# Kernel tuning notes

Measured on AMD Instinct MI355X. Metric: run time of the kernel, lower is better.

Reference implementation:

```python
import jax, jax.numpy as jnp
import numpy as np

SOLVER_STEPS = 4  # fixed-step Euler steps per ODE solve (solver_step)


def setup_inputs() -> dict:
    key = jax.random.key(0)
    ks = jax.random.split(key, 10)
    B, T, D, H = 256, 1024, 128, 512
    sd = 1.0 / np.sqrt(H)
    n = lambda k, shape, scale: (jax.random.normal(k, shape, jnp.float32) * scale)
    return {
        "x": n(ks[0], (B, T, D), 1.0),
        "t": jax.random.uniform(ks[1], (B, T, 1), jnp.float32),
        # torch.nn.LSTMCell parameters (gate order: input, forget, cell, output)
        "W_ih": n(ks[2], (4 * H, D), sd),
        "W_hh": n(ks[3], (4 * H, H), sd),
        "b_ih": n(ks[4], (4 * H,), sd),
        "b_hh": n(ks[5], (4 * H,), sd),
        # DiffeqConcat drift MLP: (H+1) -> H -> H, Tanh activation
        "w1": n(ks[6], (H, H + 1), 1.0 / np.sqrt(H + 1)),
        "b1": n(ks[7], (H,), 0.01),
        "w2": n(ks[8], (H, H), sd),
        "b2": n(ks[9], (H,), 0.01),
    }


def _drift(y, s, w1, b1, w2, b2):
    # MLP(concat([s, y])): s is the (scalar) integration time in [0, 1]
    inp = jnp.concatenate([jnp.full_like(y[..., :1], s), y], axis=-1)
    return jnp.tanh(inp @ w1.T + b1) @ w2.T + b2


def _ode_evolve(h, t_i, w1, b1, w2, b2):
    # Integrate dy/ds = t_i * f(s, y) for s in [0, 1] with fixed-step Euler
    # (torchdiffeq time-rescaling trick used by ODEModel/DiffeqConcat).
    dt = 1.0 / SOLVER_STEPS
    y = h
    for k in range(SOLVER_STEPS):
        y = y + dt * t_i * _drift(y, k * dt, w1, b1, w2, b2)  # t_i: (B,1) broadcasts
    return y


def _lstm_cell(x_i, c, h, W_ih, W_hh, b_ih, b_hh):
    gates = x_i @ W_ih.T + b_ih + h @ W_hh.T + b_hh  # (B, 4H)
    i, f, g, o = jnp.split(gates, 4, axis=-1)
    c_new = jax.nn.sigmoid(f) * c + jax.nn.sigmoid(i) * jnp.tanh(g)
    h_new = jax.nn.sigmoid(o) * jnp.tanh(c_new)
    return c_new, h_new


def reference(x, t, W_ih, W_hh, b_ih, b_hh, w1, b1, w2, b2):
    B, T, D = x.shape
    H = W_hh.shape[1]

    def step(carry, inp):
        c, h = carry
        x_i, t_i = inp  # (B, D), (B, 1)
        h_pre = _ode_evolve(h, t_i, w1, b1, w2, b2)
        c, h = _lstm_cell(x_i, c, h, W_ih, W_hh, b_ih, b_hh)
        return (c, h), h_pre

    init = (jnp.zeros((B, H), x.dtype), jnp.zeros((B, H), x.dtype))
    xs = (jnp.swapaxes(x, 0, 1), jnp.swapaxes(t, 0, 1))  # time-major for scan
    _, hiddens = jax.lax.scan(step, init, xs)  # (T, B, H)
    return jnp.swapaxes(hiddens, 0, 1)  # (B, T, H)
```

## Files before the change

### kernel.cpp

```cpp
#include <hip/hip_runtime.h>
#include <stdint.h>

#define B_  256
#define T_  1024
#define D_  128
#define H_  512
#define G4_ 2048
#define BT_ (B_ * T_)

#define NG_  16
#define NCW_ 8

typedef unsigned short u16;
typedef __attribute__((ext_vector_type(8))) short    bf16x8;
typedef __attribute__((ext_vector_type(8))) u16      u16x8;
typedef __attribute__((ext_vector_type(4))) float    f32x4;
typedef __attribute__((ext_vector_type(4))) uint32_t u32x4;

static __device__ __forceinline__ u16 f2bf(float f) {
  uint32_t u = __builtin_bit_cast(uint32_t, f);
  u += 0x7FFFu + ((u >> 16) & 1u);
  return (u16)(u >> 16);
}

static __device__ __forceinline__ u16x8 pack8(float4 a, float4 b) {
  u16x8 p;
  p[0] = f2bf(a.x); p[1] = f2bf(a.y); p[2] = f2bf(a.z); p[3] = f2bf(a.w);
  p[4] = f2bf(b.x); p[5] = f2bf(b.y); p[6] = f2bf(b.z); p[7] = f2bf(b.w);
  return p;
}

static __device__ __forceinline__ float fast_sig(float x) {
  return 1.f / (1.f + __expf(-x));
}
static __device__ __forceinline__ float fast_tanh(float x) {
  return 1.f - 2.f / (__expf(2.f * x) + 1.f);
}

__global__ void prep_kernel(const float* __restrict__ Whh, const float* __restrict__ Wih,
                            const float* __restrict__ w1,  const float* __restrict__ w2,
                            const float* __restrict__ b_ih, const float* __restrict__ b_hh,
                            u16* __restrict__ Whh_bf, u16* __restrict__ Wih_bf,
                            u16* __restrict__ w1y_bf, u16* __restrict__ w2_bf,
                            float* __restrict__ w1s, float* __restrict__ bsum,
                            uint32_t* __restrict__ xch32, float* __restrict__ Yd) {
  const int idx = blockIdx.x * blockDim.x + threadIdx.x;
  if (idx < G4_ * H_) Whh_bf[idx] = f2bf(Whh[idx]);
  if (idx < G4_ * D_) Wih_bf[idx] = f2bf(Wih[idx]);
  if (idx < H_ * H_) {
    const int n = idx >> 9, k = idx & 511;
    w1y_bf[idx] = f2bf(w1[n * 513 + 1 + k]);
    w2_bf[idx]  = f2bf(w2[idx]);
  }
  if (idx < H_)  w1s[idx]  = w1[idx * 513];
  if (idx < G4_) bsum[idx] = b_ih[idx] + b_hh[idx];
  if (idx < 2 * B_ * H_) xch32[idx] = 0;
  if (idx < B_ * H_) {
    const int b = idx >> 9, h = idx & 511;
    Yd[(size_t)b * T_ * H_ + h] = 0.f;
  }
}

__global__ void xconv_kernel(const float* __restrict__ x, u16* __restrict__ xbf) {
  const size_t i = ((size_t)blockIdx.x * blockDim.x + threadIdx.x) * 16;
  const float4* s4 = (const float4*)(x + i);
  float4 a = s4[0], b = s4[1], c = s4[2], d = s4[3];
  *(u16x8*)(xbf + i)     = pack8(a, b);
  *(u16x8*)(xbf + i + 8) = pack8(c, d);
}

__launch_bounds__(256, 1)
__global__ void lstm_persist5(const u16* __restrict__ xbf,
                              const u16* __restrict__ Whh_bf,
                              const u16* __restrict__ Wih_bf,
                              const float* __restrict__ bsum,
                              float* __restrict__ Yd,
                              uint32_t* __restrict__ xch32) {
  __shared__ u16 As[16][648];

  const int tid  = threadIdx.x;
  const int lane = tid & 63;
  const int wv   = tid >> 6;
  const int bid  = blockIdx.x;
  const int g    = bid & 15;
  const int cw   = bid >> 4;
  const int br0  = g * 16;

  const int cl = lane & 15;
  const int ko = (lane >> 4) * 8;
  const int jb = cw * 64 + wv * 16 + cl;

  bf16x8 wf[4][20];
#pragma unroll
  for (int gt = 0; gt < 4; ++gt) {
    const size_t j0 = (size_t)(gt * H_ + jb);
#pragma unroll
    for (int kt = 0; kt < 16; ++kt)
      wf[gt][kt] = *(const bf16x8*)(Whh_bf + j0 * H_ + kt * 32 + ko);
#pragma unroll
    for (int kt = 0; kt < 4; ++kt)
      wf[gt][16 + kt] = *(const bf16x8*)(Wih_bf + j0 * D_ + kt * 32 + ko);
  }
#pragma unroll
  for (int gt = 0; gt < 4; ++gt)
#pragma unroll
    for (int kt = 0; kt < 20; ++kt)
      asm volatile("" : "+v"(wf[gt][kt]));

  const int row0 = (lane >> 4) * 4;
  float cst[4] = {0.f, 0.f, 0.f, 0.f};
  const float bi  = bsum[jb];
  const float bff = bsum[H_ + jb];
  const float bgg = bsum[2 * H_ + jb];
  const float boo = bsum[3 * H_ + jb];

  const int prow = tid >> 4;
  const int pcb  = (tid & 15) * 32;
  const u16* xrow = xbf + (size_t)(br0 + (tid >> 4)) * T_ * D_ + (tid & 15) * 8;

  for (int s = 0; s < T_ - 1; ++s) {
    const u16x8 xa = *(const u16x8*)(xrow + (size_t)s * D_);

    if (s == 0) {
      u16x8 z = {};
#pragma unroll
      for (int i = 0; i < 4; ++i) *(u16x8*)&As[prow][pcb + i * 8] = z;
    } else {
      const char* base = (const char*)(xch32 + (((size_t)(s & 1) * NG_ + g) << 13)) + tid * 128;
      const uint32_t want = (uint32_t)s;
      u32x4 r0, r1, r2, r3, r4, r5, r6, r7;
      bool ok;
      do {
        asm volatile(
          "global_load_dwordx4 %0, %8, off sc0 sc1\n\t"
          "global_load_dwordx4 %1, %8, off offset:16 sc0 sc1\n\t"
          "global_load_dwordx4 %2, %8, off offset:32 sc0 sc1\n\t"
          "global_load_dwordx4 %3, %8, off offset:48 sc0 sc1\n\t"
          "global_load_dwordx4 %4, %8, off offset:64 sc0 sc1\n\t"
          "global_load_dwordx4 %5, %8, off offset:80 sc0 sc1\n\t"
          "global_load_dwordx4 %6, %8, off offset:96 sc0 sc1\n\t"
          "global_load_dwordx4 %7, %8, off offset:112 sc0 sc1\n\t"
          "s_waitcnt vmcnt(0)"
          : "=&v"(r0), "=&v"(r1), "=&v"(r2), "=&v"(r3),
            "=&v"(r4), "=&v"(r5), "=&v"(r6), "=&v"(r7)
          : "v"(base) : "memory");
        ok = true;
#pragma unroll
        for (int i = 0; i < 4; ++i) {
          ok = ok && ((r0[i] & 0xFFFFu) == want) && ((r1[i] & 0xFFFFu) == want)
                  && ((r2[i] & 0xFFFFu) == want) && ((r3[i] & 0xFFFFu) == want)
                  && ((r4[i] & 0xFFFFu) == want) && ((r5[i] & 0xFFFFu) == want)
                  && ((r6[i] & 0xFFFFu) == want) && ((r7[i] & 0xFFFFu) == want);
        }
      } while (!ok);
      u16x8 d0, d1, d2, d3;
#pragma unroll
      for (int i = 0; i < 4; ++i) {
        d0[i] = (u16)(r0[i] >> 16); d0[4 + i] = (u16)(r1[i] >> 16);
        d1[i] = (u16)(r2[i] >> 16); d1[4 + i] = (u16)(r3[i] >> 16);
        d2[i] = (u16)(r4[i] >> 16); d2[4 + i] = (u16)(r5[i] >> 16);
        d3[i] = (u16)(r6[i] >> 16); d3[4 + i] = (u16)(r7[i] >> 16);
      }
      *(u16x8*)&As[prow][pcb]      = d0;
      *(u16x8*)&As[prow][pcb + 8]  = d1;
      *(u16x8*)&As[prow][pcb + 16] = d2;
      *(u16x8*)&As[prow][pcb + 24] = d3;
    }
    *(u16x8*)&As[tid >> 4][512 + (tid & 15) * 8] = xa;
    __syncthreads();

    f32x4 a0 = {}, a1 = {}, a2 = {}, a3 = {};
#pragma unroll
    for (int kt = 0; kt < 20; ++kt) {
      bf16x8 a = *(const bf16x8*)&As[cl][kt * 32 + ko];
      a0 = __builtin_amdgcn_mfma_f32_16x16x32_bf16(a, wf[0][kt], a0, 0, 0, 0);
      a1 = __builtin_amdgcn_mfma_f32_16x16x32_bf16(a, wf[1][kt], a1, 0, 0, 0);
      a2 = __builtin_amdgcn_mfma_f32_16x16x32_bf16(a, wf[2][kt], a2, 0, 0, 0);
      a3 = __builtin_amdgcn_mfma_f32_16x16x32_bf16(a, wf[3][kt], a3, 0, 0, 0);
    }

    {
      const uint32_t tag = (uint32_t)(s + 1);
      uint32_t* xdst = xch32 + (((size_t)((s + 1) & 1) * NG_ + g) << 13) + row0 * 512 + jb;
      float*    ydst = Yd + ((size_t)(br0 + row0) * T_ + (s + 1)) * H_ + jb;
#pragma unroll
      for (int r = 0; r < 4; ++r) {
        const float gi = a0[r] + bi;
        const float gf = a1[r] + bff;
        const float gg = a2[r] + bgg;
        const float go = a3[r] + boo;
        cst[r] = fast_sig(gf) * cst[r] + fast_sig(gi) * fast_tanh(gg);
        const float h = fast_sig(go) * fast_tanh(cst[r]);
        const uint32_t wd = ((uint32_t)f2bf(h) << 16) | tag;
        asm volatile("global_store_dword %0, %1, off sc0 sc1"
                     :: "v"(xdst + r * 512), "v"(wd) : "memory");
        ydst[(size_t)r * T_ * H_] = h;
      }
    }
    __syncthreads();
  }
}

__launch_bounds__(512)
__global__ void ode_fused2(const float* __restrict__ tptr,
                           const u16* __restrict__ w1y,
                           const u16* __restrict__ w2v,
                           const float* __restrict__ b1,
                           const float* __restrict__ b2,
                           const float* __restrict__ w1s,
                           float* __restrict__ Yd) {
  __shared__ u16 At[64][520];

  const int tid  = threadIdx.x;
  const int lane = tid & 63;
  const int wv   = tid >> 6;
  const int n0w  = wv * 64;
  const size_t m0 = (size_t)blockIdx.x * 64;
  const int cl = lane & 15;
  const int rq = (lane >> 4) * 4;
  const int ko = (lane >> 4) * 8;

  float b1v[4], b2v[4], w1sv[4];
#pragma unroll
  for (int nf = 0; nf < 4; ++nf) {
    const int cg = n0w + nf * 16 + cl;
    b1v[nf] = b1[cg]; b2v[nf] = b2[cg]; w1sv[nf] = w1s[cg];
  }
  float tv[4][4];
#pragma unroll
  for (int mf = 0; mf < 4; ++mf)
#pragma unroll
    for (int r = 0; r < 4; ++r)
      tv[mf][r] = 0.25f * tptr[m0 + mf * 16 + rq + r];

  f32x4 Y[4][4];
#pragma unroll
  for (int mf = 0; mf < 4; ++mf)
#pragma unroll
    for (int nf = 0; nf < 4; ++nf)
#pragma unroll
      for (int r = 0; r < 4; ++r)
        Y[mf][nf][r] = Yd[(m0 + mf * 16 + rq + r) * 512 + n0w + nf * 16 + cl];

#define WRITE_AT(EXPR)                                                        \
  do {                                                                        \
    _Pragma("unroll") for (int mf = 0; mf < 4; ++mf)                          \
    _Pragma("unroll") for (int nf = 0; nf < 4; ++nf)                          \
    _Pragma("unroll") for (int r = 0; r < 4; ++r)                             \
      At[mf * 16 + rq + r][n0w + nf * 16 + cl] = f2bf(EXPR);                  \
  } while (0)

#define GEMM_DIRECT(WPTR, ACC)                                                \
  do {                                                                        \
    _Pragma("unroll 2") for (int cc = 0; cc < 16; ++cc) {                     \
      bf16x8 bfv[4], af[4];                                                   \
      _Pragma("unroll") for (int nf = 0; nf < 4; ++nf)                        \
        bfv[nf] = *(const bf16x8*)((WPTR) + (size_t)(n0w + nf * 16 + cl) * 512\
                                   + cc * 32 + ko);                           \
      _Pragma("unroll") for (int mf = 0; mf < 4; ++mf)                        \
        af[mf] = *(const bf16x8*)&At[mf * 16 + cl][cc * 32 + ko];             \
      _Pragma("unroll") for (int mf = 0; mf < 4; ++mf)                        \
      _Pragma("unroll") for (int nf = 0; nf < 4; ++nf)                        \
        ACC[mf][nf] = __builtin_amdgcn_mfma_f32_16x16x32_bf16(                \
            af[mf], bfv[nf], ACC[mf][nf], 0, 0, 0);                           \
    }                                                                         \
  } while (0)

  WRITE_AT(Y[mf][nf][r]);
  __syncthreads();

#pragma unroll 1
  for (int k = 0; k < 4; ++k) {
    const float sk = 0.25f * k;
    f32x4 acc[4][4] = {};
    GEMM_DIRECT(w1y, acc);
    __syncthreads();
    WRITE_AT(fast_tanh(acc[mf][nf][r] + b1v[nf] + sk * w1sv[nf]));
    __syncthreads();
    f32x4 acc2[4][4] = {};
    GEMM_DIRECT(w2v, acc2);
    __syncthreads();
#pragma unroll
    for (int mf = 0; mf < 4; ++mf)
#pragma unroll
      for (int nf = 0; nf < 4; ++nf)
#pragma unroll
        for (int r = 0; r < 4; ++r)
          Y[mf][nf][r] += tv[mf][r] * (acc2[mf][nf][r] + b2v[nf]);
    if (k < 3) {
      WRITE_AT(Y[mf][nf][r]);
      __syncthreads();
    }
  }
#undef GEMM_DIRECT
#undef WRITE_AT

#pragma unroll
  for (int mf = 0; mf < 4; ++mf)
#pragma unroll
    for (int nf = 0; nf < 4; ++nf)
#pragma unroll
      for (int r = 0; r < 4; ++r)
        Yd[(m0 + mf * 16 + rq + r) * 512 + n0w + nf * 16 + cl] = Y[mf][nf][r];
}

extern "C" void kernel_launch(void* const* d_in, const int* in_sizes, int n_in,
                              void* d_out, int out_size, void* d_ws, size_t ws_size,
                              hipStream_t stream) {
  const float* x    = (const float*)d_in[0];
  const float* t    = (const float*)d_in[1];
  const float* W_ih = (const float*)d_in[2];
  const float* W_hh = (const float*)d_in[3];
  const float* b_ih = (const float*)d_in[4];
  const float* b_hh = (const float*)d_in[5];
  const float* w1   = (const float*)d_in[6];
  const float* b1   = (const float*)d_in[7];
  const float* w2   = (const float*)d_in[8];
  const float* b2   = (const float*)d_in[9];
  float* Yd = (float*)d_out;

  char* ws = (char*)d_ws;
  size_t off = 0;
  auto alloc = [&](size_t bytes) {
    void* p = ws + off;
    off += (bytes + 255) & ~(size_t)255;
    return p;
  };
  u16*      Whh_bf = (u16*)alloc((size_t)G4_ * H_ * 2);
  u16*      Wih_bf = (u16*)alloc((size_t)G4_ * D_ * 2);
  u16*      w1y_bf = (u16*)alloc((size_t)H_ * H_ * 2);
  u16*      w2_bf  = (u16*)alloc((size_t)H_ * H_ * 2);
  float*    w1s    = (float*)alloc(H_ * 4);
  float*    bsum   = (float*)alloc(G4_ * 4);
  uint32_t* xch32  = (uint32_t*)alloc((size_t)2 * B_ * H_ * 4);
  u16*      xbf    = (u16*)alloc((size_t)BT_ * D_ * 2);

  prep_kernel<<<4096, 256, 0, stream>>>(W_hh, W_ih, w1, w2, b_ih, b_hh,
                                        Whh_bf, Wih_bf, w1y_bf, w2_bf, w1s, bsum, xch32, Yd);
  xconv_kernel<<<8192, 256, 0, stream>>>(x, xbf);

  lstm_persist5<<<dim3(NG_ * NCW_), 256, 0, stream>>>(xbf, Whh_bf, Wih_bf, bsum, Yd, xch32);

  ode_fused2<<<dim3(BT_ / 64), 512, 0, stream>>>(t, w1y_bf, w2_bf, b1, b2, w1s, Yd);
}
```

Before: 6.912 ms.

## Duplicate hidden-state exchange into L2-scoped and system-scoped buffers for faster polling

Each LSTM block now writes its tagged hidden state twice: once with an sc0-only store (intended to stay coherent at the local L2/XCD level) and once with an sc0 sc1 store to a second buffer. Consumers poll the sc0-only buffer, which is meant to be cheaper per probe, and every fourth failed spin fall back to the system-coherent copy so cross-XCD producers are still observed. The aim is to cut the latency of the per-step inter-block handoff in the persistent recurrence. The cost is doubled exchange stores and a second workspace buffer. It also depends on the coherence semantics of the cache-scope bits, because peers on another XCD may only be seen through the fallback path.

```diff
diff --git a/kernel.cpp b/kernel.cpp
--- a/kernel.cpp
+++ b/kernel.cpp
@@ -43,7 +43,8 @@
                             u16* __restrict__ Whh_bf, u16* __restrict__ Wih_bf,
                             u16* __restrict__ w1y_bf, u16* __restrict__ w2_bf,
                             float* __restrict__ w1s, float* __restrict__ bsum,
-                            uint32_t* __restrict__ xch32, float* __restrict__ Yd) {
+                            uint32_t* __restrict__ xchL, uint32_t* __restrict__ xchM,
+                            float* __restrict__ Yd) {
   const int idx = blockIdx.x * blockDim.x + threadIdx.x;
   if (idx < G4_ * H_) Whh_bf[idx] = f2bf(Whh[idx]);
   if (idx < G4_ * D_) Wih_bf[idx] = f2bf(Wih[idx]);
@@ -54,7 +55,7 @@
   }
   if (idx < H_)  w1s[idx]  = w1[idx * 513];
   if (idx < G4_) bsum[idx] = b_ih[idx] + b_hh[idx];
-  if (idx < 2 * B_ * H_) xch32[idx] = 0;
+  if (idx < 2 * B_ * H_) { xchL[idx] = 0; xchM[idx] = 0; }
   if (idx < B_ * H_) {
     const int b = idx >> 9, h = idx & 511;
     Yd[(size_t)b * T_ * H_ + h] = 0.f;
@@ -70,12 +71,13 @@
 }
 
 __launch_bounds__(256, 1)
-__global__ void lstm_persist5(const u16* __restrict__ xbf,
+__global__ void lstm_persist6(const u16* __restrict__ xbf,
                               const u16* __restrict__ Whh_bf,
                               const u16* __restrict__ Wih_bf,
                               const float* __restrict__ bsum,
                               float* __restrict__ Yd,
-                              uint32_t* __restrict__ xch32) {
+                              uint32_t* __restrict__ xchL,
+                              uint32_t* __restrict__ xchM) {
   __shared__ u16 As[16][648];
 
   const int tid  = threadIdx.x;
@@ -126,24 +128,27 @@
 #pragma unroll
       for (int i = 0; i < 4; ++i) *(u16x8*)&As[prow][pcb + i * 8] = z;
     } else {
-      const char* base = (const char*)(xch32 + (((size_t)(s & 1) * NG_ + g) << 13)) + tid * 128;
+      const size_t blk = ((size_t)(s & 1) * NG_ + g) << 13;
+      const char* baseL = (const char*)(xchL + blk) + tid * 128;
+      const char* baseM = (const char*)(xchM + blk) + tid * 128;
       const uint32_t want = (uint32_t)s;
       u32x4 r0, r1, r2, r3, r4, r5, r6, r7;
-      bool ok;
+      bool ok = false;
+      int spin = 0;
       do {
         asm volatile(
-          "global_load_dwordx4 %0, %8, off sc0 sc1\n\t"
-          "global_load_dwordx4 %1, %8, off offset:16 sc0 sc1\n\t"
-          "global_load_dwordx4 %2, %8, off offset:32 sc0 sc1\n\t"
-          "global_load_dwordx4 %3, %8, off offset:48 sc0 sc1\n\t"
-          "global_load_dwordx4 %4, %8, off offset:64 sc0 sc1\n\t"
-          "global_load_dwordx4 %5, %8, off offset:80 sc0 sc1\n\t"
-          "global_load_dwordx4 %6, %8, off offset:96 sc0 sc1\n\t"
-          "global_load_dwordx4 %7, %8, off offset:112 sc0 sc1\n\t"
+          "global_load_dwordx4 %0, %8, off sc0\n\t"
+          "global_load_dwordx4 %1, %8, off offset:16 sc0\n\t"
+          "global_load_dwordx4 %2, %8, off offset:32 sc0\n\t"
+          "global_load_dwordx4 %3, %8, off offset:48 sc0\n\t"
+          "global_load_dwordx4 %4, %8, off offset:64 sc0\n\t"
+          "global_load_dwordx4 %5, %8, off offset:80 sc0\n\t"
+          "global_load_dwordx4 %6, %8, off offset:96 sc0\n\t"
+          "global_load_dwordx4 %7, %8, off offset:112 sc0\n\t"
           "s_waitcnt vmcnt(0)"
           : "=&v"(r0), "=&v"(r1), "=&v"(r2), "=&v"(r3),
             "=&v"(r4), "=&v"(r5), "=&v"(r6), "=&v"(r7)
-          : "v"(base) : "memory");
+          : "v"(baseL) : "memory");
         ok = true;
 #pragma unroll
         for (int i = 0; i < 4; ++i) {
@@ -151,6 +156,29 @@
                   && ((r2[i] & 0xFFFFu) == want) && ((r3[i] & 0xFFFFu) == want)
                   && ((r4[i] & 0xFFFFu) == want) && ((r5[i] & 0xFFFFu) == want)
                   && ((r6[i] & 0xFFFFu) == want) && ((r7[i] & 0xFFFFu) == want);
+        }
+        if (!ok && ((spin++ & 3) == 3)) {
+          asm volatile(
+            "global_load_dwordx4 %0, %8, off sc0 sc1\n\t"
+            "global_load_dwordx4 %1, %8, off offset:16 sc0 sc1\n\t"
+            "global_load_dwordx4 %2, %8, off offset:32 sc0 sc1\n\t"
+            "global_load_dwordx4 %3, %8, off offset:48 sc0 sc1\n\t"
+            "global_load_dwordx4 %4, %8, off offset:64 sc0 sc1\n\t"
+            "global_load_dwordx4 %5, %8, off offset:80 sc0 sc1\n\t"
+            "global_load_dwordx4 %6, %8, off offset:96 sc0 sc1\n\t"
+            "global_load_dwordx4 %7, %8, off offset:112 sc0 sc1\n\t"
+            "s_waitcnt vmcnt(0)"
+            : "=&v"(r0), "=&v"(r1), "=&v"(r2), "=&v"(r3),
+              "=&v"(r4), "=&v"(r5), "=&v"(r6), "=&v"(r7)
+            : "v"(baseM) : "memory");
+          ok = true;
+#pragma unroll
+          for (int i = 0; i < 4; ++i) {
+            ok = ok && ((r0[i] & 0xFFFFu) == want) && ((r1[i] & 0xFFFFu) == want)
+                    && ((r2[i] & 0xFFFFu) == want) && ((r3[i] & 0xFFFFu) == want)
+                    && ((r4[i] & 0xFFFFu) == want) && ((r5[i] & 0xFFFFu) == want)
+                    && ((r6[i] & 0xFFFFu) == want) && ((r7[i] & 0xFFFFu) == want);
+          }
         }
       } while (!ok);
       u16x8 d0, d1, d2, d3;
@@ -181,7 +209,9 @@
 
     {
       const uint32_t tag = (uint32_t)(s + 1);
-      uint32_t* xdst = xch32 + (((size_t)((s + 1) & 1) * NG_ + g) << 13) + row0 * 512 + jb;
+      const size_t nblk = ((size_t)((s + 1) & 1) * NG_ + g) << 13;
+      uint32_t* dL = xchL + nblk + row0 * 512 + jb;
+      uint32_t* dM = xchM + nblk + row0 * 512 + jb;
       float*    ydst = Yd + ((size_t)(br0 + row0) * T_ + (s + 1)) * H_ + jb;
 #pragma unroll
       for (int r = 0; r < 4; ++r) {
@@ -192,8 +222,9 @@
         cst[r] = fast_sig(gf) * cst[r] + fast_sig(gi) * fast_tanh(gg);
         const float h = fast_sig(go) * fast_tanh(cst[r]);
         const uint32_t wd = ((uint32_t)f2bf(h) << 16) | tag;
-        asm volatile("global_store_dword %0, %1, off sc0 sc1"
-                     :: "v"(xdst + r * 512), "v"(wd) : "memory");
+        asm volatile("global_store_dword %0, %2, off sc0\n\t"
+                     "global_store_dword %1, %2, off sc0 sc1"
+                     :: "v"(dL + r * 512), "v"(dM + r * 512), "v"(wd) : "memory");
         ydst[(size_t)r * T_ * H_] = h;
       }
     }
@@ -332,14 +363,17 @@
   u16*      w2_bf  = (u16*)alloc((size_t)H_ * H_ * 2);
   float*    w1s    = (float*)alloc(H_ * 4);
   float*    bsum   = (float*)alloc(G4_ * 4);
-  uint32_t* xch32  = (uint32_t*)alloc((size_t)2 * B_ * H_ * 4);
+  uint32_t* xchL   = (uint32_t*)alloc((size_t)2 * B_ * H_ * 4);
+  uint32_t* xchM   = (uint32_t*)alloc((size_t)2 * B_ * H_ * 4);
   u16*      xbf    = (u16*)alloc((size_t)BT_ * D_ * 2);
 
   prep_kernel<<<4096, 256, 0, stream>>>(W_hh, W_ih, w1, w2, b_ih, b_hh,
-                                        Whh_bf, Wih_bf, w1y_bf, w2_bf, w1s, bsum, xch32, Yd);
+                                        Whh_bf, Wih_bf, w1y_bf, w2_bf, w1s, bsum,
+                                        xchL, xchM, Yd);
   xconv_kernel<<<8192, 256, 0, stream>>>(x, xbf);
 
-  lstm_persist5<<<dim3(NG_ * NCW_), 256, 0, stream>>>(xbf, Whh_bf, Wih_bf, bsum, Yd, xch32);
+  lstm_persist6<<<dim3(NG_ * NCW_), 256, 0, stream>>>(xbf, Whh_bf, Wih_bf, bsum, Yd,
+                                                      xchL, xchM);
 
   ode_fused2<<<dim3(BT_ / 64), 512, 0, stream>>>(t, w1y_bf, w2_bf, b1, b2, w1s, Yd);
 }
```

Result: slower. 7.970 ms (+15.3%).

## Interleave four batch groups per LSTM block with double-buffered LDS exchange

Applied to the files above, without the earlier changes.

The persistent LSTM kernel now launches 32 blocks instead of 128. Each block cycles round-robin through four independent 16-row batch groups within every timestep. While the MFMA gate computation runs on one group, the block issues the x load and the cross-block hidden-state poll for the next group, using a double-buffered LDS tile. This aims to hide the global-memory flag-polling and exchange latency of the sequential recurrence behind useful work, at the cost of four times more serial compute per block and far fewer active CUs.

```diff
diff --git a/kernel.cpp b/kernel.cpp
--- a/kernel.cpp
+++ b/kernel.cpp
@@ -9,7 +9,6 @@
 #define BT_ (B_ * T_)
 
 #define NG_  16
-#define NCW_ 8
 
 typedef unsigned short u16;
 typedef __attribute__((ext_vector_type(8))) short    bf16x8;
@@ -70,21 +69,21 @@
 }
 
 __launch_bounds__(256, 1)
-__global__ void lstm_persist5(const u16* __restrict__ xbf,
+__global__ void lstm_persist7(const u16* __restrict__ xbf,
                               const u16* __restrict__ Whh_bf,
                               const u16* __restrict__ Wih_bf,
                               const float* __restrict__ bsum,
                               float* __restrict__ Yd,
                               uint32_t* __restrict__ xch32) {
-  __shared__ u16 As[16][648];
+  __shared__ u16 As[2][16][648];
 
   const int tid  = threadIdx.x;
   const int lane = tid & 63;
   const int wv   = tid >> 6;
   const int bid  = blockIdx.x;
-  const int g    = bid & 15;
-  const int cw   = bid >> 4;
-  const int br0  = g * 16;
+  const int mg   = bid & 3;
+  const int cw   = bid >> 2;
+  const int mg4  = mg * 4;
 
   const int cl = lane & 15;
   const int ko = (lane >> 4) * 8;
@@ -108,7 +107,7 @@
       asm volatile("" : "+v"(wf[gt][kt]));
 
   const int row0 = (lane >> 4) * 4;
-  float cst[4] = {0.f, 0.f, 0.f, 0.f};
+  f32x4 cst0 = {}, cst1 = {}, cst2 = {}, cst3 = {};
   const float bi  = bsum[jb];
   const float bff = bsum[H_ + jb];
   const float bgg = bsum[2 * H_ + jb];
@@ -116,89 +115,143 @@
 
   const int prow = tid >> 4;
   const int pcb  = (tid & 15) * 32;
-  const u16* xrow = xbf + (size_t)(br0 + (tid >> 4)) * T_ * D_ + (tid & 15) * 8;
+  const u16* xb[4];
+#pragma unroll
+  for (int q = 0; q < 4; ++q)
+    xb[q] = xbf + (size_t)((mg4 + q) * 16 + (tid >> 4)) * T_ * D_ + (tid & 15) * 8;
+
+  int cb = 0;
+
+  {
+    u16x8 z = {};
+#pragma unroll
+    for (int i = 0; i < 4; ++i) *(u16x8*)&As[0][prow][pcb + i * 8] = z;
+    *(u16x8*)&As[0][tid >> 4][512 + (tid & 15) * 8] = *(const u16x8*)xb[0];
+  }
+  __syncthreads();
+
+#define CHECK_TAGS(OK, WANT)                                                  \
+  do {                                                                        \
+    OK = true;                                                                \
+    _Pragma("unroll") for (int i = 0; i < 4; ++i) {                           \
+      OK = OK && ((r0[i] & 0xFFFFu) == (WANT)) && ((r1[i] & 0xFFFFu) == (WANT)) \
+              && ((r2[i] & 0xFFFFu) == (WANT)) && ((r3[i] & 0xFFFFu) == (WANT)) \
+              && ((r4[i] & 0xFFFFu) == (WANT)) && ((r5[i] & 0xFFFFu) == (WANT)) \
+              && ((r6[i] & 0xFFFFu) == (WANT)) && ((r7[i] & 0xFFFFu) == (WANT)); \
+    }                                                                         \
+  } while (0)
+
+#define SLOT(Q, CSTV)                                                         \
+  {                                                                           \
+    const int gq = mg4 + (Q);                                                 \
+    const bool have_next = !((Q) == 3 && s == T_ - 2);                        \
+    const int ns = ((Q) < 3) ? s : (s + 1);                                   \
+    const int gn = ((Q) < 3) ? (mg4 + (Q) + 1) : mg4;                         \
+    const bool need_poll = have_next && (ns > 0);                             \
+    u32x4 r0, r1, r2, r3, r4, r5, r6, r7;                                     \
+    u16x8 xa = {};                                                            \
+    const char* nb = (const char*)(xch32 +                                    \
+        (((size_t)(ns & 1) * NG_ + gn) << 13)) + tid * 128;                   \
+    if (have_next)                                                            \
+      xa = *(const u16x8*)(xb[((Q) + 1) & 3] + (size_t)ns * D_);              \
+    if (need_poll) {                                                          \
+      asm volatile(                                                           \
+        "global_load_dwordx4 %0, %8, off sc0 sc1\n\t"                         \
+        "global_load_dwordx4 %1, %8, off offset:16 sc0 sc1\n\t"               \
+        "global_load_dwordx4 %2, %8, off offset:32 sc0 sc1\n\t"               \
+        "global_load_dwordx4 %3, %8, off offset:48 sc0 sc1\n\t"               \
+        "global_load_dwordx4 %4, %8, off offset:64 sc0 sc1\n\t"               \
+        "global_load_dwordx4 %5, %8, off offset:80 sc0 sc1\n\t"               \
+        "global_load_dwordx4 %6, %8, off offset:96 sc0 sc1\n\t"               \
+        "global_load_dwordx4 %7, %8, off offset:112 sc0 sc1"                  \
+        : "=&v"(r0), "=&v"(r1), "=&v"(r2), "=&v"(r3),                         \
+          "=&v"(r4), "=&v"(r5), "=&v"(r6), "=&v"(r7)                          \
+        : "v"(nb) : "memory");                                                \
+    }                                                                         \
+                      \
+    f32x4 a0 = {}, a1 = {}, a2 = {}, a3 = {};                                 \
+    _Pragma("unroll") for (int kt = 0; kt < 20; ++kt) {                       \
+      bf16x8 a = *(const bf16x8*)&As[cb][cl][kt * 32 + ko];                   \
+      a0 = __builtin_amdgcn_mfma_f32_16x16x32_bf16(a, wf[0][kt], a0, 0, 0, 0);\
+      a1 = __builtin_amdgcn_mfma_f32_16x16x32_bf16(a, wf[1][kt], a1, 0, 0, 0);\
+      a2 = __builtin_amdgcn_mfma_f32_16x16x32_bf16(a, wf[2][kt], a2, 0, 0, 0);\
+      a3 = __builtin_amdgcn_mfma_f32_16x16x32_bf16(a, wf[3][kt], a3, 0, 0, 0);\
+    }                                                                         \
+    if (need_poll) {                                                          \
+      asm volatile("s_waitcnt vmcnt(0)"                                       \
+        : "+v"(r0), "+v"(r1), "+v"(r2), "+v"(r3),                             \
+          "+v"(r4), "+v"(r5), "+v"(r6), "+v"(r7) :: "memory");                \
+      const uint32_t want = (uint32_t)ns;                                     \
+      bool ok; CHECK_TAGS(ok, want);                                          \
+      while (!ok) {                                                           \
+        asm volatile(                                                         \
+          "global_load_dwordx4 %0, %8, off sc0 sc1\n\t"                       \
+          "global_load_dwordx4 %1, %8, off offset:16 sc0 sc1\n\t"             \
+          "global_load_dwordx4 %2, %8, off offset:32 sc0 sc1\n\t"             \
+          "global_load_dwordx4 %3, %8, off offset:48 sc0 sc1\n\t"             \
+          "global_load_dwordx4 %4, %8, off offset:64 sc0 sc1\n\t"             \
+          "global_load_dwordx4 %5, %8, off offset:80 sc0 sc1\n\t"             \
+          "global_load_dwordx4 %6, %8, off offset:96 sc0 sc1\n\t"             \
+          "global_load_dwordx4 %7, %8, off offset:112 sc0 sc1\n\t"            \
+          "s_waitcnt vmcnt(0)"                                                \
+          : "=&v"(r0), "=&v"(r1), "=&v"(r2), "=&v"(r3),                       \
+            "=&v"(r4), "=&v"(r5), "=&v"(r6), "=&v"(r7)                        \
+          : "v"(nb) : "memory");                                              \
+        CHECK_TAGS(ok, want);                                                 \
+      }                                                                       \
+    }                                                                         \
+               \
+    {                                                                         \
+      const uint32_t tag = (uint32_t)(s + 1);                                 \
+      uint32_t* dM = xch32 + (((size_t)((s + 1) & 1) * NG_ + gq) << 13)       \
+                     + row0 * 512 + jb;                                       \
+      float* ydst = Yd + ((size_t)(gq * 16 + row0) * T_ + (s + 1)) * H_ + jb; \
+      _Pragma("unroll") for (int r = 0; r < 4; ++r) {                         \
+        const float gi = a0[r] + bi;                                          \
+        const float gf = a1[r] + bff;                                         \
+        const float gg = a2[r] + bgg;                                         \
+        const float go = a3[r] + boo;                                         \
+        CSTV[r] = fast_sig(gf) * CSTV[r] + fast_sig(gi) * fast_tanh(gg);      \
+        const float h = fast_sig(go) * fast_tanh(CSTV[r]);                    \
+        const uint32_t wd = ((uint32_t)f2bf(h) << 16) | tag;                  \
+        asm volatile("global_store_dword %0, %1, off sc0 sc1"                 \
+                     :: "v"(dM + r * 512), "v"(wd) : "memory");               \
+        ydst[(size_t)r * T_ * H_] = h;                                        \
+      }                                                                       \
+    }                                                                         \
+    __syncthreads();       \
+    if (have_next) {                                                          \
+      if (ns == 0) {                                                          \
+        u16x8 z = {};                                                         \
+        _Pragma("unroll") for (int i = 0; i < 4; ++i)                         \
+          *(u16x8*)&As[cb ^ 1][prow][pcb + i * 8] = z;                        \
+      } else {                                                                \
+        u16x8 d0, d1, d2, d3;                                                 \
+        _Pragma("unroll") for (int i = 0; i < 4; ++i) {                       \
+          d0[i] = (u16)(r0[i] >> 16); d0[4 + i] = (u16)(r1[i] >> 16);         \
+          d1[i] = (u16)(r2[i] >> 16); d1[4 + i] = (u16)(r3[i] >> 16);         \
+          d2[i] = (u16)(r4[i] >> 16); d2[4 + i] = (u16)(r5[i] >> 16);         \
+          d3[i] = (u16)(r6[i] >> 16); d3[4 + i] = (u16)(r7[i] >> 16);         \
+        }                                                                     \
+        *(u16x8*)&As[cb ^ 1][prow][pcb]      = d0;                            \
+        *(u16x8*)&As[cb ^ 1][prow][pcb + 8]  = d1;                            \
+        *(u16x8*)&As[cb ^ 1][prow][pcb + 16] = d2;                            \
+        *(u16x8*)&As[cb ^ 1][prow][pcb + 24] = d3;                            \
+      }                                                                       \
+      *(u16x8*)&As[cb ^ 1][tid >> 4][512 + (tid & 15) * 8] = xa;              \
+    }                                                                         \
+    __syncthreads();                  \
+    cb ^= 1;                                                                  \
+  }
 
   for (int s = 0; s < T_ - 1; ++s) {
-    const u16x8 xa = *(const u16x8*)(xrow + (size_t)s * D_);
-
-    if (s == 0) {
-      u16x8 z = {};
-#pragma unroll
-      for (int i = 0; i < 4; ++i) *(u16x8*)&As[prow][pcb + i * 8] = z;
-    } else {
-      const char* base = (const char*)(xch32 + (((size_t)(s & 1) * NG_ + g) << 13)) + tid * 128;
-      const uint32_t want = (uint32_t)s;
-      u32x4 r0, r1, r2, r3, r4, r5, r6, r7;
-      bool ok;
-      do {
-        asm volatile(
-          "global_load_dwordx4 %0, %8, off sc0 sc1\n\t"
-          "global_load_dwordx4 %1, %8, off offset:16 sc0 sc1\n\t"
-          "global_load_dwordx4 %2, %8, off offset:32 sc0 sc1\n\t"
-          "global_load_dwordx4 %3, %8, off offset:48 sc0 sc1\n\t"
-          "global_load_dwordx4 %4, %8, off offset:64 sc0 sc1\n\t"
-          "global_load_dwordx4 %5, %8, off offset:80 sc0 sc1\n\t"
-          "global_load_dwordx4 %6, %8, off offset:96 sc0 sc1\n\t"
-          "global_load_dwordx4 %7, %8, off offset:112 sc0 sc1\n\t"
-          "s_waitcnt vmcnt(0)"
-          : "=&v"(r0), "=&v"(r1), "=&v"(r2), "=&v"(r3),
-            "=&v"(r4), "=&v"(r5), "=&v"(r6), "=&v"(r7)
-          : "v"(base) : "memory");
-        ok = true;
-#pragma unroll
-        for (int i = 0; i < 4; ++i) {
-          ok = ok && ((r0[i] & 0xFFFFu) == want) && ((r1[i] & 0xFFFFu) == want)
-                  && ((r2[i] & 0xFFFFu) == want) && ((r3[i] & 0xFFFFu) == want)
-                  && ((r4[i] & 0xFFFFu) == want) && ((r5[i] & 0xFFFFu) == want)
-                  && ((r6[i] & 0xFFFFu) == want) && ((r7[i] & 0xFFFFu) == want);
-        }
-      } while (!ok);
-      u16x8 d0, d1, d2, d3;
-#pragma unroll
-      for (int i = 0; i < 4; ++i) {
-        d0[i] = (u16)(r0[i] >> 16); d0[4 + i] = (u16)(r1[i] >> 16);
-        d1[i] = (u16)(r2[i] >> 16); d1[4 + i] = (u16)(r3[i] >> 16);
-        d2[i] = (u16)(r4[i] >> 16); d2[4 + i] = (u16)(r5[i] >> 16);
-        d3[i] = (u16)(r6[i] >> 16); d3[4 + i] = (u16)(r7[i] >> 16);
-      }
-      *(u16x8*)&As[prow][pcb]      = d0;
-      *(u16x8*)&As[prow][pcb + 8]  = d1;
-      *(u16x8*)&As[prow][pcb + 16] = d2;
-      *(u16x8*)&As[prow][pcb + 24] = d3;
-    }
-    *(u16x8*)&As[tid >> 4][512 + (tid & 15) * 8] = xa;
-    __syncthreads();
-
-    f32x4 a0 = {}, a1 = {}, a2 = {}, a3 = {};
-#pragma unroll
-    for (int kt = 0; kt < 20; ++kt) {
-      bf16x8 a = *(const bf16x8*)&As[cl][kt * 32 + ko];
-      a0 = __builtin_amdgcn_mfma_f32_16x16x32_bf16(a, wf[0][kt], a0, 0, 0, 0);
-      a1 = __builtin_amdgcn_mfma_f32_16x16x32_bf16(a, wf[1][kt], a1, 0, 0, 0);
-      a2 = __builtin_amdgcn_mfma_f32_16x16x32_bf16(a, wf[2][kt], a2, 0, 0, 0);
-      a3 = __builtin_amdgcn_mfma_f32_16x16x32_bf16(a, wf[3][kt], a3, 0, 0, 0);
-    }
-
-    {
-      const uint32_t tag = (uint32_t)(s + 1);
-      uint32_t* xdst = xch32 + (((size_t)((s + 1) & 1) * NG_ + g) << 13) + row0 * 512 + jb;
-      float*    ydst = Yd + ((size_t)(br0 + row0) * T_ + (s + 1)) * H_ + jb;
-#pragma unroll
-      for (int r = 0; r < 4; ++r) {
-        const float gi = a0[r] + bi;
-        const float gf = a1[r] + bff;
-        const float gg = a2[r] + bgg;
-        const float go = a3[r] + boo;
-        cst[r] = fast_sig(gf) * cst[r] + fast_sig(gi) * fast_tanh(gg);
-        const float h = fast_sig(go) * fast_tanh(cst[r]);
-        const uint32_t wd = ((uint32_t)f2bf(h) << 16) | tag;
-        asm volatile("global_store_dword %0, %1, off sc0 sc1"
-                     :: "v"(xdst + r * 512), "v"(wd) : "memory");
-        ydst[(size_t)r * T_ * H_] = h;
-      }
-    }
-    __syncthreads();
-  }
+    SLOT(0, cst0)
+    SLOT(1, cst1)
+    SLOT(2, cst2)
+    SLOT(3, cst3)
+  }
+#undef SLOT
+#undef CHECK_TAGS
 }
 
 __launch_bounds__(512)
@@ -336,10 +389,11 @@
   u16*      xbf    = (u16*)alloc((size_t)BT_ * D_ * 2);
 
   prep_kernel<<<4096, 256, 0, stream>>>(W_hh, W_ih, w1, w2, b_ih, b_hh,
-                                        Whh_bf, Wih_bf, w1y_bf, w2_bf, w1s, bsum, xch32, Yd);
+                                        Whh_bf, Wih_bf, w1y_bf, w2_bf, w1s, bsum,
+                                        xch32, Yd);
   xconv_kernel<<<8192, 256, 0, stream>>>(x, xbf);
 
-  lstm_persist5<<<dim3(NG_ * NCW_), 256, 0, stream>>>(xbf, Whh_bf, Wih_bf, bsum, Yd, xch32);
+  lstm_persist7<<<dim3(32), 256, 0, stream>>>(xbf, Whh_bf, Wih_bf, bsum, Yd, xch32);
 
   ode_fused2<<<dim3(BT_ / 64), 512, 0, stream>>>(t, w1y_bf, w2_bf, b1, b2, w1s, Yd);
 }
```

Result: slower. 20.44 ms (+195.7%).

## Stage LSTM hidden outputs in LDS and publish coalesced per-block exchange slices

Applied to the files above, without the earlier changes.

Each block now writes its new hidden values with tags into a shared-memory buffer. After a barrier it publishes them as one coalesced dwordx4 store per thread into a per-block slice of the exchange buffer, instead of issuing scattered dword stores. A block's own slice is read back from LDS rather than polled from global memory, and __syncthreads is swapped for a raw lgkmcnt wait plus s_barrier. The Yd output is now written from the bf16-truncated hidden value, which lowers precision of the stored h, and the added barrier-then-publish stage sits on the recurrent critical path.

```diff
diff --git a/kernel.cpp b/kernel.cpp
--- a/kernel.cpp
+++ b/kernel.cpp
@@ -36,6 +36,8 @@
 static __device__ __forceinline__ float fast_tanh(float x) {
   return 1.f - 2.f / (__expf(2.f * x) + 1.f);
 }
+
+#define BAR_LDS() asm volatile("s_waitcnt lgkmcnt(0)\n\ts_barrier" ::: "memory")
 
 __global__ void prep_kernel(const float* __restrict__ Whh, const float* __restrict__ Wih,
                             const float* __restrict__ w1,  const float* __restrict__ w2,
@@ -70,13 +72,14 @@
 }
 
 __launch_bounds__(256, 1)
-__global__ void lstm_persist5(const u16* __restrict__ xbf,
+__global__ void lstm_persist8(const u16* __restrict__ xbf,
                               const u16* __restrict__ Whh_bf,
                               const u16* __restrict__ Wih_bf,
                               const float* __restrict__ bsum,
                               float* __restrict__ Yd,
                               uint32_t* __restrict__ xch32) {
-  __shared__ u16 As[16][648];
+  __shared__ u16      As[16][648];
+  __shared__ uint32_t hb[16][68];
 
   const int tid  = threadIdx.x;
   const int lane = tid & 63;
@@ -86,9 +89,10 @@
   const int cw   = bid >> 4;
   const int br0  = g * 16;
 
-  const int cl = lane & 15;
-  const int ko = (lane >> 4) * 8;
-  const int jb = cw * 64 + wv * 16 + cl;
+  const int cl  = lane & 15;
+  const int ko  = (lane >> 4) * 8;
+  const int jcl = wv * 16 + cl;
+  const int jb  = cw * 64 + jcl;
 
   bf16x8 wf[4][20];
 #pragma unroll
@@ -114,8 +118,11 @@
   const float bgg = bsum[2 * H_ + jb];
   const float boo = bsum[3 * H_ + jb];
 
-  const int prow = tid >> 4;
-  const int pcb  = (tid & 15) * 32;
+  const int pcw   = tid >> 5;
+  const int pj    = tid & 31;
+  const int prw   = pj >> 1;
+  const int colh  = (pj & 1) * 32;
+  const bool own  = (pcw == cw);
   const u16* xrow = xbf + (size_t)(br0 + (tid >> 4)) * T_ * D_ + (tid & 15) * 8;
 
   for (int s = 0; s < T_ - 1; ++s) {
@@ -124,9 +131,24 @@
     if (s == 0) {
       u16x8 z = {};
 #pragma unroll
-      for (int i = 0; i < 4; ++i) *(u16x8*)&As[prow][pcb + i * 8] = z;
+      for (int i = 0; i < 4; ++i)
+        *(u16x8*)&As[prw][pcw * 64 + colh + i * 8] = z;
+    } else if (own) {
+#pragma unroll
+      for (int i = 0; i < 4; ++i) {
+        u32x4 a = *(const u32x4*)&hb[prw][colh + i * 8];
+        u32x4 b = *(const u32x4*)&hb[prw][colh + i * 8 + 4];
+        u16x8 d;
+#pragma unroll
+        for (int j = 0; j < 4; ++j) {
+          d[j] = (u16)(a[j] >> 16);
+          d[4 + j] = (u16)(b[j] >> 16);
+        }
+        *(u16x8*)&As[prw][pcw * 64 + colh + i * 8] = d;
+      }
     } else {
-      const char* base = (const char*)(xch32 + (((size_t)(s & 1) * NG_ + g) << 13)) + tid * 128;
+      const char* nb = (const char*)xch32 +
+          ((((size_t)(s & 1) * NG_ + g) * NCW_ + pcw) << 12) + pj * 128;
       const uint32_t want = (uint32_t)s;
       u32x4 r0, r1, r2, r3, r4, r5, r6, r7;
       bool ok;
@@ -143,7 +165,7 @@
           "s_waitcnt vmcnt(0)"
           : "=&v"(r0), "=&v"(r1), "=&v"(r2), "=&v"(r3),
             "=&v"(r4), "=&v"(r5), "=&v"(r6), "=&v"(r7)
-          : "v"(base) : "memory");
+          : "v"(nb) : "memory");
         ok = true;
 #pragma unroll
         for (int i = 0; i < 4; ++i) {
@@ -161,13 +183,14 @@
         d2[i] = (u16)(r4[i] >> 16); d2[4 + i] = (u16)(r5[i] >> 16);
         d3[i] = (u16)(r6[i] >> 16); d3[4 + i] = (u16)(r7[i] >> 16);
       }
-      *(u16x8*)&As[prow][pcb]      = d0;
-      *(u16x8*)&As[prow][pcb + 8]  = d1;
-      *(u16x8*)&As[prow][pcb + 16] = d2;
-      *(u16x8*)&As[prow][pcb + 24] = d3;
+      const int cb = pcw * 64 + colh;
+      *(u16x8*)&As[prw][cb]      = d0;
+      *(u16x8*)&As[prw][cb + 8]  = d1;
+      *(u16x8*)&As[prw][cb + 16] = d2;
+      *(u16x8*)&As[prw][cb + 24] = d3;
     }
     *(u16x8*)&As[tid >> 4][512 + (tid & 15) * 8] = xa;
-    __syncthreads();
+    BAR_LDS();
 
     f32x4 a0 = {}, a1 = {}, a2 = {}, a3 = {};
 #pragma unroll
@@ -181,8 +204,6 @@
 
     {
       const uint32_t tag = (uint32_t)(s + 1);
-      uint32_t* xdst = xch32 + (((size_t)((s + 1) & 1) * NG_ + g) << 13) + row0 * 512 + jb;
-      float*    ydst = Yd + ((size_t)(br0 + row0) * T_ + (s + 1)) * H_ + jb;
 #pragma unroll
       for (int r = 0; r < 4; ++r) {
         const float gi = a0[r] + bi;
@@ -191,13 +212,25 @@
         const float go = a3[r] + boo;
         cst[r] = fast_sig(gf) * cst[r] + fast_sig(gi) * fast_tanh(gg);
         const float h = fast_sig(go) * fast_tanh(cst[r]);
-        const uint32_t wd = ((uint32_t)f2bf(h) << 16) | tag;
-        asm volatile("global_store_dword %0, %1, off sc0 sc1"
-                     :: "v"(xdst + r * 512), "v"(wd) : "memory");
-        ydst[(size_t)r * T_ * H_] = h;
+        hb[row0 + r][jcl] = ((uint32_t)f2bf(h) << 16) | tag;
       }
     }
-    __syncthreads();
+    BAR_LDS();
+
+    {
+      const int pr2 = tid >> 4, pc4 = (tid & 15) * 4;
+      u32x4 pub = *(const u32x4*)&hb[pr2][pc4];
+      char* dst = (char*)xch32 +
+          ((((size_t)((s + 1) & 1) * NG_ + g) * NCW_ + cw) << 12) + tid * 16;
+      asm volatile("global_store_dwordx4 %0, %1, off sc0 sc1"
+                   :: "v"(dst), "v"(pub) : "memory");
+      u32x4 yv;
+#pragma unroll
+      for (int j = 0; j < 4; ++j) yv[j] = pub[j] & 0xFFFF0000u;
+      float* yd = Yd + ((size_t)(br0 + pr2) * T_ + (s + 1)) * H_ + cw * 64 + pc4;
+      asm volatile("global_store_dwordx4 %0, %1, off"
+                   :: "v"(yd), "v"(yv) : "memory");
+    }
   }
 }
 
@@ -336,10 +369,11 @@
   u16*      xbf    = (u16*)alloc((size_t)BT_ * D_ * 2);
 
   prep_kernel<<<4096, 256, 0, stream>>>(W_hh, W_ih, w1, w2, b_ih, b_hh,
-                                        Whh_bf, Wih_bf, w1y_bf, w2_bf, w1s, bsum, xch32, Yd);
+                                        Whh_bf, Wih_bf, w1y_bf, w2_bf, w1s, bsum,
+                                        xch32, Yd);
   xconv_kernel<<<8192, 256, 0, stream>>>(x, xbf);
 
-  lstm_persist5<<<dim3(NG_ * NCW_), 256, 0, stream>>>(xbf, Whh_bf, Wih_bf, bsum, Yd, xch32);
+  lstm_persist8<<<dim3(NG_ * NCW_), 256, 0, stream>>>(xbf, Whh_bf, Wih_bf, bsum, Yd, xch32);
 
   ode_fused2<<<dim3(BT_ / 64), 512, 0, stream>>>(t, w1y_bf, w2_bf, b1, b2, w1s, Yd);
 }
```

Measured after the change: 7.276 ms. 5.3% more time.
